# Optimization experiments

Measured on AMD Instinct MI355X. Metric: run time of the kernel, lower is better.

## Reference

```python
import jax, jax.numpy as jnp
import numpy as np

# irreps_in = 128x0e + 64x1o + 32x2e
MUL0, MUL1, MUL2 = 128, 64, 32
L1_DIM, L2_DIM = 3, 5
D0, D1, D2 = MUL0, MUL1 * L1_DIM, MUL2 * L2_DIM  # 128, 192, 160
DIM = D0 + D1 + D2                               # 480
H, Z = 64, 64
N = 16384
# fully-connected tensor-product fan-in normalization (paths: 0e*0e, 1o*1o, 2e*2e -> 0e)
ALPHA = 1.0 / np.sqrt(MUL0 * MUL0 + MUL1 * MUL1 + MUL2 * MUL2)


def setup_inputs() -> dict:
    key = jax.random.key(0)
    ks = jax.random.split(key, 8)
    return {
        "tensor_in": jax.random.normal(ks[0], (N, DIM), dtype=jnp.float32),
        "W0": jax.random.normal(ks[1], (MUL0, MUL0, H), dtype=jnp.float32),
        "W1": jax.random.normal(ks[2], (MUL1, MUL1, H), dtype=jnp.float32),
        "W2": jax.random.normal(ks[3], (MUL2, MUL2, H), dtype=jnp.float32),
        "w1": jax.random.normal(ks[4], (H, H), dtype=jnp.float32) / np.sqrt(H),
        "b1": jnp.zeros((H,), dtype=jnp.float32),
        "w2": jax.random.normal(ks[5], (H, Z), dtype=jnp.float32) / np.sqrt(H),
        "b2": jnp.zeros((Z,), dtype=jnp.float32),
        "w3": jax.random.normal(ks[6], (Z, Z), dtype=jnp.float32) / np.sqrt(Z),
        "b3": jnp.zeros((Z,), dtype=jnp.float32),
    }


def _fctp_mlp(t, W0, W1, W2, w1, b1, w2, b2, w3, b3):
    # split flat irreps vector into (mul, 2l+1) blocks
    x0 = t[:, :D0]                                   # [N, 128]    l=0
    x1 = t[:, D0:D0 + D1].reshape(-1, MUL1, L1_DIM)  # [N, 64, 3]  l=1
    x2 = t[:, D0 + D1:].reshape(-1, MUL2, L2_DIM)    # [N, 32, 5]  l=2
    # CG contraction l x l -> 0e: normalized dot over m, weighted mix over (u, v)
    h = ALPHA * (
        jnp.einsum('nu,nv,uvh->nh', x0, x0, W0)
        + jnp.einsum('num,nvm,uvh->nh', x1, x1, W1) / np.sqrt(3.0)
        + jnp.einsum('num,nvm,uvh->nh', x2, x2, W2) / np.sqrt(5.0)
    )
    h = jax.nn.silu(h @ w1 + b1)
    h = jax.nn.silu(h @ w2 + b2)
    return h @ w3 + b3                                # [N, Z]


def reference(tensor_in, W0, W1, W2, w1, b1, w2, b2, w3, b3):
    f = lambda t: _fctp_mlp(t, W0, W1, W2, w1, b1, w2, b2, w3, b3)
    x, vjp_fn = jax.vjp(f, tensor_in)
    (y,) = vjp_fn(jnp.ones_like(x))  # autograd.grad(x, tensor_in, ones_like(x))
    return x, y
```

## Files before the change

kernel.cpp:

```cpp
#include <hip/hip_runtime.h>
#include <hip/hip_bf16.h>
#include <hip/hip_fp16.h>

typedef short    bf16x8 __attribute__((ext_vector_type(8)));
typedef _Float16 f16x8  __attribute__((ext_vector_type(8)));
typedef _Float16 f16x2v __attribute__((ext_vector_type(2)));
typedef float    f32x4  __attribute__((ext_vector_type(4)));

#define DEVI __device__ __forceinline__

static constexpr int    NSAMP = 16384;
static constexpr int    TDIM  = 480;
static constexpr int    KTOT  = 21504;

static constexpr size_t SZ_B   = (size_t)KTOT * 64 * 2;
static constexpr size_t O_GWS  = 0;
static constexpr size_t O_BFWD = 0;
static constexpr size_t O_HPRE = O_BFWD + SZ_B;
static constexpr size_t O_BBWD = (size_t)TDIM * NSAMP * 4;
static constexpr size_t O_DH   = O_BBWD + SZ_B;
static constexpr size_t O_W1T  = O_DH   + (size_t)NSAMP*64*2;
static constexpr size_t O_W2T  = O_W1T + (size_t)64*64*4;
static constexpr size_t O_W3T  = O_W2T + (size_t)64*64*4;

DEVI float b2f(unsigned short s) { union { unsigned u; float f; } v; v.u = (unsigned)s << 16; return v.f; }
DEVI unsigned short f2b(float f) { union { __hip_bfloat16 h; unsigned short s; } v; v.h = __float2bfloat16(f); return v.s; }
DEVI unsigned short f2h(float f) { union { __half h; unsigned short s; } v; v.h = __float2half(f); return v.s; }
DEVI float h2f(unsigned short s) { union { unsigned short s; _Float16 h; } v; v.s = s; return (float)v.h; }
DEVI bf16x8 as_bf(uint4 q) { union { uint4 q; bf16x8 v; } u; u.q = q; return u.v; }
DEVI f16x8  as_f16(uint4 q) { union { uint4 q; f16x8 v; } u; u.q = q; return u.v; }
DEVI f32x4 mfma16(bf16x8 a, bf16x8 b, f32x4 c) { return __builtin_amdgcn_mfma_f32_16x16x32_bf16(a, b, c, 0, 0, 0); }
DEVI f32x4 mfma16h(f16x8 a, f16x8 b, f32x4 c)  { return __builtin_amdgcn_mfma_f32_16x16x32_f16 (a, b, c, 0, 0, 0); }
DEVI unsigned pkmul(unsigned a, unsigned b) {
  union { unsigned u; __half2 h; } x, y, r;
  x.u = a; y.u = b; r.h = __hmul2(x.h, y.h); return r.u;
}
DEVI unsigned pk_f16(float a, float b) {
  auto r = __builtin_amdgcn_cvt_pkrtz(a, b);
  union { decltype(r) h; unsigned u; } v;
  v.h = r; return v.u;
}
DEVI float fmix_lo(float a, unsigned w, float c) {
  float d = c;
  asm("v_fma_mix_f32 %0, %1, %2, %0 op_sel_hi:[0,1,0]" : "+v"(d) : "v"(a), "v"(w));
  return d;
}
DEVI float fmix_hi(float a, unsigned w, float c) {
  float d = c;
  asm("v_fma_mix_f32 %0, %1, %2, %0 op_sel:[0,1,0] op_sel_hi:[0,1,0]" : "+v"(d) : "v"(a), "v"(w));
  return d;
}

template<int NQ>
DEVI unsigned wsel4(const uint4 (&q)[NQ], int wi) {
  const uint4 qq = q[wi>>2];
  const int k = wi&3;
  return k==0?qq.x: k==1?qq.y: k==2?qq.z: qq.w;
}
template<int NQ>
DEVI float h16_at(const uint2 (&q)[NQ], int e) {
  const uint2 qq = q[e>>2];
  const unsigned w = ((e>>1)&1) ? qq.y : qq.x;
  const f16x2v p = __builtin_bit_cast(f16x2v, w);
  return (float)p[e&1];
}

template<int R> struct RC;
template<> struct RC<0> { static constexpr int COLS=128, OFF=0,   STRIDE=136, ROWS=128, NCH=4, NM=1, CBASE=0,   KBASE=0,    OUT=0;   };
template<> struct RC<1> { static constexpr int COLS=192, OFF=128, STRIDE=200, ROWS=64,  NCH=2, NM=3, CBASE=512, KBASE=1024, OUT=128; };
template<> struct RC<2> { static constexpr int COLS=160, OFF=320, STRIDE=168, ROWS=32,  NCH=1, NM=5, CBASE=640, KBASE=1280, OUT=320; };

__global__ __launch_bounds__(256) void k_prep(
    const float* __restrict__ W0, const float* __restrict__ W1, const float* __restrict__ W2,
    const float* __restrict__ w1, const float* __restrict__ w2, const float* __restrict__ w3,
    unsigned short* __restrict__ bfwd, unsigned short* __restrict__ bbwd,
    float* __restrict__ w1t, float* __restrict__ w2t, float* __restrict__ w3t)
{
  const int e = blockIdx.x*256 + threadIdx.x;
  const float CA = 0.0068192924f;
  const float C1 = 0.0039371205f;
  const float C2 = 0.0030496940f;
  if (e < KTOT*64) {
    {
      int j = e & 7, lane = (e>>3)&63, hf = (e>>9)&3, chunk = e>>11;
      int k = chunk*32 + (lane>>4)*8 + j;
      int h = hf*16 + (lane&15);
      float v;
      if (k < 16384)      v = CA * W0[(size_t)k*64 + h];
      else if (k < 20480) v = C1 * W1[(size_t)(k-16384)*64 + h];
      else                v = C2 * W2[(size_t)(k-20480)*64 + h];
      bfwd[e] = f2h(v);
    }
    {
      int j = e & 7, lane = (e>>3)&63, kc = (e>>9)&1, kb = e>>10;
      int k = kb*16 + (lane&15);
      int h = kc*32 + (lane>>4)*8 + j;
      float v;
      if (k < 16384)      { int u=k>>7,    vv=k&127;          v = CA*(W0[(size_t)(u*128+vv)*64+h] + W0[(size_t)(vv*128+u)*64+h]); }
      else if (k < 20480) { int l=k-16384; int u=l>>6, vv=l&63; v = C1*(W1[(size_t)(u*64+vv)*64+h] + W1[(size_t)(vv*64+u)*64+h]); }
      else                { int l=k-20480; int u=l>>5, vv=l&31; v = C2*(W2[(size_t)(u*32+vv)*64+h] + W2[(size_t)(vv*32+u)*64+h]); }
      bbwd[e] = f2b(v);
    }
  }
  if (e < 4096) {
    int i = e>>6, j = e&63;
    w1t[j*64+i] = w1[e]; w2t[j*64+i] = w2[e]; w3t[j*64+i] = w3[e];
  }
}

template<int R, bool H>
DEVI void load_tile(const float* __restrict__ t, int nb, unsigned short* lx)
{
  const int tid = threadIdx.x;
  const int s = tid >> 2, p = tid & 3;
  constexpr int CH = RC<R>::COLS/4;
  const float4* src = reinterpret_cast<const float4*>(t + (size_t)(nb+s)*TDIM + RC<R>::OFF + p*CH);
  unsigned short* dst = lx + s*RC<R>::STRIDE + p*CH;
  #pragma unroll
  for (int e4 = 0; e4 < CH/4; ++e4) {
    float4 v = src[e4];
    ushort4 o;
    if (H) { o.x = f2h(v.x); o.y = f2h(v.y); o.z = f2h(v.z); o.w = f2h(v.w); }
    else   { o.x = f2b(v.x); o.y = f2b(v.y); o.z = f2b(v.z); o.w = f2b(v.w); }
    *reinterpret_cast<ushort4*>(dst + e4*4) = o;
  }
}

DEVI void fwd_region0_f16(const unsigned short* lx, const uint4* __restrict__ bf,
                          int slot, int lane, f32x4 (&acc)[4][4])
{
  const int quad = lane>>4, col = lane&15;
  for (int u = slot; u < 128; u += 16) {
    unsigned xu2[4];
    #pragma unroll
    for (int mf = 0; mf < 4; ++mf) {
      unsigned s = lx[(mf*16+col)*136 + u];
      xu2[mf] = s | (s<<16);
    }
    #pragma unroll 1
    for (int c = 0; c < 4; ++c) {
      const int chunk = u*4 + c;
      uint4 bv[4];
      #pragma unroll
      for (int hf = 0; hf < 4; ++hf) bv[hf] = bf[(size_t)(chunk*4 + hf)*64 + lane];
      #pragma unroll
      for (int mf = 0; mf < 4; ++mf) {
        const uint4 xq = *reinterpret_cast<const uint4*>(lx + (mf*16+col)*136 + c*32 + quad*8);
        uint4 afq;
        afq.x = pkmul(xu2[mf], xq.x);
        afq.y = pkmul(xu2[mf], xq.y);
        afq.z = pkmul(xu2[mf], xq.z);
        afq.w = pkmul(xu2[mf], xq.w);
        #pragma unroll
        for (int hf = 0; hf < 4; ++hf)
          acc[mf][hf] = mfma16h(as_f16(afq), as_f16(bv[hf]), acc[mf][hf]);
      }
    }
  }
}

template<int R>
DEVI void fwd_region_f16(const unsigned short* lx, const uint4* __restrict__ bf,
                         int slot, int lane, f32x4 (&acc)[4][4])
{
  constexpr int NM = RC<R>::NM;
  const int quad = lane>>4, col = lane&15;
  for (int u = slot; u < RC<R>::ROWS; u += 16) {
    #pragma unroll 1
    for (int c = 0; c < RC<R>::NCH; ++c) {
      const int chunk = RC<R>::CBASE + u*RC<R>::NCH + c;
      uint4 bv[4];
      #pragma unroll
      for (int hf = 0; hf < 4; ++hf) bv[hf] = bf[(size_t)(chunk*4 + hf)*64 + lane];
      #pragma unroll
      for (int mf = 0; mf < 4; ++mf) {
        const unsigned short* rowp = lx + (mf*16+col)*RC<R>::STRIDE;
        float xu[NM];
        #pragma unroll
        for (int m = 0; m < NM; ++m) xu[m] = h2f(rowp[u*NM + m]);
        uint4 xq[NM];
        const uint4* xp4 = reinterpret_cast<const uint4*>(rowp + (c*32 + quad*8)*NM);
        #pragma unroll
        for (int q = 0; q < NM; ++q) xq[q] = xp4[q];
        unsigned aw[4];
        #pragma unroll
        for (int jp = 0; jp < 4; ++jp) {
          float p0 = 0.f, p1 = 0.f;
          #pragma unroll
          for (int m = 0; m < NM; ++m) {
            const int e0 = (2*jp+0)*NM + m, e1 = (2*jp+1)*NM + m;
            const unsigned w0 = wsel4(xq, e0>>1);
            const unsigned w1v = wsel4(xq, e1>>1);
            p0 = (e0&1) ? fmix_hi(xu[m], w0,  p0) : fmix_lo(xu[m], w0,  p0);
            p1 = (e1&1) ? fmix_hi(xu[m], w1v, p1) : fmix_lo(xu[m], w1v, p1);
          }
          aw[jp] = pk_f16(p0, p1);
        }
        uint4 afq; afq.x = aw[0]; afq.y = aw[1]; afq.z = aw[2]; afq.w = aw[3];
        #pragma unroll
        for (int hf = 0; hf < 4; ++hf)
          acc[mf][hf] = mfma16h(as_f16(afq), as_f16(bv[hf]), acc[mf][hf]);
      }
    }
  }
}

__global__ __launch_bounds__(256,2) void k_fwd(const float* __restrict__ t,
                                               const uint4* __restrict__ bfwd,
                                               float* __restrict__ hpre)
{
  __shared__ __align__(16) unsigned char smem[25600];
  unsigned short* lx = (unsigned short*)smem;
  const int nb = blockIdx.x*64;
  const int wv = threadIdx.x>>6, lane = threadIdx.x&63;
  const int slot = blockIdx.y*4 + wv;
  const int quad = lane>>4, col = lane&15;

  f32x4 acc[4][4];
  #pragma unroll
  for (int a = 0; a < 4; ++a)
    #pragma unroll
    for (int b = 0; b < 4; ++b) acc[a][b] = (f32x4){0.f,0.f,0.f,0.f};

  load_tile<0,true>(t, nb, lx); __syncthreads();
  fwd_region0_f16(lx, bfwd, slot, lane, acc); __syncthreads();
  load_tile<1,true>(t, nb, lx); __syncthreads();
  fwd_region_f16<1>(lx, bfwd, slot, lane, acc); __syncthreads();
  load_tile<2,true>(t, nb, lx); __syncthreads();
  fwd_region_f16<2>(lx, bfwd, slot, lane, acc); __syncthreads();

  float* red = (float*)smem;
  for (int tw = 0; tw < 4; ++tw) {
    if (wv == tw) {
      #pragma unroll
      for (int mf = 0; mf < 4; ++mf)
        #pragma unroll
        for (int hf = 0; hf < 4; ++hf)
          #pragma unroll
          for (int rr = 0; rr < 4; ++rr) {
            int idx = (mf*16 + quad*4 + rr)*64 + hf*16 + col;
            if (tw == 0) red[idx] = acc[mf][hf][rr]; else red[idx] += acc[mf][hf][rr];
          }
    }
    __syncthreads();
  }
  float* hp = hpre + (size_t)blockIdx.y*NSAMP*64;
  for (int i = threadIdx.x; i < 4096; i += 256)
    hp[(size_t)(nb + (i>>6))*64 + (i&63)] = red[i];
}

__global__ __launch_bounds__(256) void k_mlp(
    const float* __restrict__ hpre,
    const float* __restrict__ w1, const float* __restrict__ b1,
    const float* __restrict__ w2, const float* __restrict__ b2,
    const float* __restrict__ w3, const float* __restrict__ b3,
    const float* __restrict__ w1t, const float* __restrict__ w2t, const float* __restrict__ w3t,
    float* __restrict__ xout, unsigned short* __restrict__ dhb)
{
  __shared__ float Hs[64*65];
  __shared__ float Bh1[64*64];
  __shared__ float Bh2[64*64];
  __shared__ float Bg2[64*64];
  __shared__ unsigned short Bsp1[64*64];
  const int n  = threadIdx.x & 63;
  const int wv = threadIdx.x >> 6;
  const int jb = __builtin_amdgcn_readfirstlane(wv*16);
  const int nb = blockIdx.x*64;
  const size_t row = (size_t)(nb + n)*64;
  const size_t base = (size_t)nb*64;

  for (int idx = threadIdx.x; idx < 4096; idx += 256) {
    float s = hpre[base + idx]
            + hpre[(size_t)NSAMP*64   + base + idx]
            + hpre[(size_t)2*NSAMP*64 + base + idx]
            + hpre[(size_t)3*NSAMP*64 + base + idx];
    Hs[(idx>>6)*65 + (idx&63)] = s;
  }
  __syncthreads();

  float h[64];
  #pragma unroll
  for (int i = 0; i < 64; ++i) h[i] = Hs[n*65 + i];

  float dh2r[16];
  #pragma unroll
  for (int jj = 0; jj < 16; ++jj) {
    int j = jb + jj; float s = 0.f;
    #pragma unroll
    for (int z = 0; z < 64; ++z) s += w3[j*64+z];
    dh2r[jj] = s;
  }
  #pragma unroll
  for (int jj = 0; jj < 16; ++jj) {
    int j = jb + jj; float a = b1[j];
    #pragma unroll
    for (int i = 0; i < 64; ++i) a += h[i]*w1t[j*64+i];
    float sg = 1.f/(1.f + __expf(-a));
    Bh1[j*64+n] = a*sg;
    Bsp1[j*64+n] = f2b(sg*(1.f + a*(1.f-sg)));
  }
  __syncthreads();
  float h1[64];
  #pragma unroll
  for (int i = 0; i < 64; ++i) h1[i] = Bh1[i*64+n];
  #pragma unroll
  for (int jj = 0; jj < 16; ++jj) {
    int j = jb + jj; float a = b2[j];
    #pragma unroll
    for (int i = 0; i < 64; ++i) a += h1[i]*w2t[j*64+i];
    float sg = 1.f/(1.f + __expf(-a));
    Bh2[j*64+n] = a*sg;
    Bg2[j*64+n] = dh2r[jj]*(sg*(1.f + a*(1.f-sg)));
  }
  __syncthreads();
  float h2[64];
  #pragma unroll
  for (int i = 0; i < 64; ++i) h2[i] = Bh2[i*64+n];
  #pragma unroll
  for (int jj = 0; jj < 16; ++jj) {
    int j = jb + jj; float a = b3[j];
    #pragma unroll
    for (int i = 0; i < 64; ++i) a += h2[i]*w3t[j*64+i];
    xout[row + j] = a;
  }
  float g2[64];
  #pragma unroll
  for (int i = 0; i < 64; ++i) g2[i] = Bg2[i*64+n];
  #pragma unroll
  for (int jj = 0; jj < 16; ++jj) {
    int i = jb + jj; float a = 0.f;
    #pragma unroll
    for (int z = 0; z < 64; ++z) a += g2[z]*w2[i*64+z];
    Bh1[i*64+n] = a * b2f(Bsp1[i*64+n]);
  }
  __syncthreads();
  float g1[64];
  #pragma unroll
  for (int i = 0; i < 64; ++i) g1[i] = Bh1[i*64+n];
  #pragma unroll
  for (int jj = 0; jj < 16; ++jj) {
    int i = jb + jj; float a = 0.f;
    #pragma unroll
    for (int z = 0; z < 64; ++z) a += g1[z]*w1[i*64+z];
    dhb[row + i] = f2b(a);
  }
}

template<int R>
DEVI void bwd_region(const unsigned short* lx, const uint4 (&bq)[4][2],
                     const uint4* __restrict__ ba, int slot, int lane,
                     float* __restrict__ gws, int nb)
{
  constexpr int NM = RC<R>::NM;
  const int quad = lane>>4, col = lane&15;
  for (int u = slot; u < RC<R>::ROWS; u += 16) {
    float gacc[4][NM];
    #pragma unroll
    for (int nf = 0; nf < 4; ++nf)
      #pragma unroll
      for (int m = 0; m < NM; ++m) gacc[nf][m] = 0.f;

    #pragma unroll 1
    for (int c = 0; c < RC<R>::NCH; ++c) {
      uint4 aq[2][2];
      #pragma unroll
      for (int kf = 0; kf < 2; ++kf)
        #pragma unroll
        for (int kc = 0; kc < 2; ++kc) {
          int kb = RC<R>::KBASE + u*(2*RC<R>::NCH) + c*2 + kf;
          aq[kf][kc] = ba[(size_t)(kb*2+kc)*64 + lane];
        }
      #pragma unroll
      for (int kf = 0; kf < 2; ++kf) {
        const int v0 = c*32 + kf*16 + quad*4;
        #pragma unroll
        for (int nf = 0; nf < 4; ++nf) {
          f32x4 a4 = (f32x4){0.f,0.f,0.f,0.f};
          a4 = mfma16(as_bf(aq[kf][0]), as_bf(bq[nf][0]), a4);
          a4 = mfma16(as_bf(aq[kf][1]), as_bf(bq[nf][1]), a4);
          const unsigned short* xp = lx + (nf*16+col)*RC<R>::STRIDE + v0*NM;
          uint2 xq[NM];
          const uint2* xp2 = reinterpret_cast<const uint2*>(xp);
          #pragma unroll
          for (int q = 0; q < NM; ++q) xq[q] = xp2[q];
          #pragma unroll
          for (int rr = 0; rr < 4; ++rr)
            #pragma unroll
            for (int m = 0; m < NM; ++m)
              gacc[nf][m] = __builtin_fmaf(a4[rr], h16_at(xq, rr*NM + m), gacc[nf][m]);
        }
      }
    }
    #pragma unroll
    for (int nf = 0; nf < 4; ++nf)
      #pragma unroll
      for (int m = 0; m < NM; ++m) {
        float v = gacc[nf][m];
        v += __shfl_down(v, 32, 64);
        v += __shfl_down(v, 16, 64);
        if (lane < 16)
          gws[(size_t)(RC<R>::OUT + u*NM + m)*NSAMP + nb + nf*16 + lane] = v;
      }
  }
}

__global__ __launch_bounds__(256,2) void k_bwd(const float* __restrict__ t,
                                               const uint4* __restrict__ bbwd,
                                               const unsigned short* __restrict__ dh,
                                               float* __restrict__ gws)
{
  __shared__ __align__(16) unsigned char smem[25600];
  unsigned short* lx = (unsigned short*)smem;
  const int nb = blockIdx.x*64;
  const int wv = threadIdx.x>>6, lane = threadIdx.x&63;
  const int slot = blockIdx.y*4 + wv;
  const int cl = lane&15, qd = lane>>4;

  uint4 bq[4][2];
  #pragma unroll
  for (int nf = 0; nf < 4; ++nf)
    #pragma unroll
    for (int kc = 0; kc < 2; ++kc)
      bq[nf][kc] = *reinterpret_cast<const uint4*>(dh + (size_t)(nb + nf*16 + cl)*64 + kc*32 + qd*8);

  load_tile<0,true>(t, nb, lx); __syncthreads();
  bwd_region<0>(lx, bq, bbwd, slot, lane, gws, nb); __syncthreads();
  load_tile<1,true>(t, nb, lx); __syncthreads();
  bwd_region<1>(lx, bq, bbwd, slot, lane, gws, nb); __syncthreads();
  load_tile<2,true>(t, nb, lx); __syncthreads();
  bwd_region<2>(lx, bq, bbwd, slot, lane, gws, nb);
}

__global__ __launch_bounds__(256) void k_tr(const float* __restrict__ gws,
                                            float* __restrict__ y)
{
  __shared__ float tile[32][481];
  const int n0 = blockIdx.x*32;
  for (int idx = threadIdx.x; idx < 480*8; idx += 256) {
    int c = idx >> 3, i4 = idx & 7;
    float4 v = reinterpret_cast<const float4*>(gws + (size_t)c*NSAMP + n0)[i4];
    tile[i4*4+0][c] = v.x; tile[i4*4+1][c] = v.y;
    tile[i4*4+2][c] = v.z; tile[i4*4+3][c] = v.w;
  }
  __syncthreads();
  for (int idx = threadIdx.x; idx < 32*120; idx += 256) {
    int s = idx/120, c4 = idx%120;
    float4 v = { tile[s][c4*4+0], tile[s][c4*4+1], tile[s][c4*4+2], tile[s][c4*4+3] };
    reinterpret_cast<float4*>(y + (size_t)(n0+s)*TDIM)[c4] = v;
  }
}

extern "C" void kernel_launch(void* const* d_in, const int* in_sizes, int n_in,
                              void* d_out, int out_size, void* d_ws, size_t ws_size,
                              hipStream_t stream) {
  (void)in_sizes; (void)n_in; (void)out_size; (void)ws_size;
  const float* t  = (const float*)d_in[0];
  const float* W0 = (const float*)d_in[1];
  const float* W1 = (const float*)d_in[2];
  const float* W2 = (const float*)d_in[3];
  const float* w1 = (const float*)d_in[4];
  const float* b1 = (const float*)d_in[5];
  const float* w2 = (const float*)d_in[6];
  const float* b2 = (const float*)d_in[7];
  const float* w3 = (const float*)d_in[8];
  const float* b3 = (const float*)d_in[9];

  char* ws = (char*)d_ws;
  float*          gws  = (float*)(ws + O_GWS);
  unsigned short* bfwd = (unsigned short*)(ws + O_BFWD);
  unsigned short* bbwd = (unsigned short*)(ws + O_BBWD);
  float*          hpre = (float*)(ws + O_HPRE);
  unsigned short* dhb  = (unsigned short*)(ws + O_DH);
  float*          w1t  = (float*)(ws + O_W1T);
  float*          w2t  = (float*)(ws + O_W2T);
  float*          w3t  = (float*)(ws + O_W3T);

  float* xout = (float*)d_out;
  float* y    = (float*)d_out + (size_t)NSAMP*64;

  k_prep<<<dim3(5376), dim3(256), 0, stream>>>(W0, W1, W2, w1, w2, w3,
                                               bfwd, bbwd, w1t, w2t, w3t);
  k_fwd <<<dim3(256,4), dim3(256), 0, stream>>>(t, (const uint4*)bfwd, hpre);
  k_mlp <<<dim3(256), dim3(256), 0, stream>>>(hpre, w1, b1, w2, b2, w3, b3,
                                              w1t, w2t, w3t, xout, dhb);
  k_bwd <<<dim3(256,4), dim3(256), 0, stream>>>(t, (const uint4*)bbwd, dhb, gws);
  k_tr  <<<dim3(512),   dim3(256), 0, stream>>>(gws, y);
}
```

Before: 370.2 us.

## Retile MLP kernel to 16 samples per block with vectorized weight loads

The per-sample MLP kernel now handles 16 samples per block instead of 64, so 1024 blocks are launched instead of 256 and more CUs are filled. Each thread computes 4 output features rather than 16 and reads weights and LDS rows with float4 loads, using a padded row-major LDS layout. The intent is to raise parallelism and cut the per-thread serial work and scalar load count of a small kernel. The cost is that each weight row is fetched redundantly by many more blocks, and the LDS access pattern changes, which may cause bank conflicts.

```diff
diff --git a/kernel.cpp b/kernel.cpp
--- a/kernel.cpp
+++ b/kernel.cpp
@@ -257,92 +257,174 @@
     const float* __restrict__ w1t, const float* __restrict__ w2t, const float* __restrict__ w3t,
     float* __restrict__ xout, unsigned short* __restrict__ dhb)
 {
-  __shared__ float Hs[64*65];
-  __shared__ float Bh1[64*64];
-  __shared__ float Bh2[64*64];
-  __shared__ float Bg2[64*64];
-  __shared__ unsigned short Bsp1[64*64];
-  const int n  = threadIdx.x & 63;
-  const int wv = threadIdx.x >> 6;
-  const int jb = __builtin_amdgcn_readfirstlane(wv*16);
-  const int nb = blockIdx.x*64;
+  constexpr int SB  = 16;
+  constexpr int LDW = 68;
+  __shared__ float Hs [SB*LDW];
+  __shared__ float Bh1[SB*LDW];
+  __shared__ float Bh2[SB*LDW];
+  __shared__ float Bg2[SB*LDW];
+  __shared__ unsigned short Bsp1[SB*LDW];
+  const int n  = threadIdx.x & 15;
+  const int g  = threadIdx.x >> 4;
+  const int jb = g*4;
+  const int nb = blockIdx.x*SB;
   const size_t row = (size_t)(nb + n)*64;
   const size_t base = (size_t)nb*64;
 
-  for (int idx = threadIdx.x; idx < 4096; idx += 256) {
+  for (int idx = threadIdx.x; idx < SB*64; idx += 256) {
     float s = hpre[base + idx]
             + hpre[(size_t)NSAMP*64   + base + idx]
             + hpre[(size_t)2*NSAMP*64 + base + idx]
             + hpre[(size_t)3*NSAMP*64 + base + idx];
-    Hs[(idx>>6)*65 + (idx&63)] = s;
+    Hs[(idx>>6)*LDW + (idx&63)] = s;
+  }
+
+  float dh2r[4];
+  #pragma unroll
+  for (int jj = 0; jj < 4; ++jj) {
+    const float4* wr = reinterpret_cast<const float4*>(w3 + (jb+jj)*64);
+    float s = 0.f;
+    #pragma unroll
+    for (int z4 = 0; z4 < 16; ++z4) { float4 v = wr[z4]; s += v.x; s += v.y; s += v.z; s += v.w; }
+    dh2r[jj] = s;
   }
   __syncthreads();
 
-  float h[64];
+  float hrow[64];
   #pragma unroll
-  for (int i = 0; i < 64; ++i) h[i] = Hs[n*65 + i];
-
-  float dh2r[16];
+  for (int i4 = 0; i4 < 16; ++i4) {
+    float4 v = *reinterpret_cast<const float4*>(&Hs[n*LDW + i4*4]);
+    hrow[i4*4+0]=v.x; hrow[i4*4+1]=v.y; hrow[i4*4+2]=v.z; hrow[i4*4+3]=v.w;
+  }
+
+  {
+    float h1v[4], spv[4];
+    #pragma unroll
+    for (int jj = 0; jj < 4; ++jj) {
+      const int j = jb + jj;
+      float a = b1[j];
+      const float4* wr = reinterpret_cast<const float4*>(w1t + j*64);
+      #pragma unroll
+      for (int i4 = 0; i4 < 16; ++i4) {
+        float4 wv = wr[i4];
+        a += hrow[i4*4+0]*wv.x; a += hrow[i4*4+1]*wv.y;
+        a += hrow[i4*4+2]*wv.z; a += hrow[i4*4+3]*wv.w;
+      }
+      float sg = 1.f/(1.f + __expf(-a));
+      h1v[jj] = a*sg;
+      spv[jj] = sg*(1.f + a*(1.f-sg));
+    }
+    float4 o; o.x=h1v[0]; o.y=h1v[1]; o.z=h1v[2]; o.w=h1v[3];
+    *reinterpret_cast<float4*>(&Bh1[n*LDW + jb]) = o;
+    ushort4 us; us.x=f2b(spv[0]); us.y=f2b(spv[1]); us.z=f2b(spv[2]); us.w=f2b(spv[3]);
+    *reinterpret_cast<ushort4*>(&Bsp1[n*LDW + jb]) = us;
+  }
+  __syncthreads();
+
+  float h1row[64];
   #pragma unroll
-  for (int jj = 0; jj < 16; ++jj) {
-    int j = jb + jj; float s = 0.f;
-    #pragma unroll
-    for (int z = 0; z < 64; ++z) s += w3[j*64+z];
-    dh2r[jj] = s;
-  }
-  #pragma unroll
-  for (int jj = 0; jj < 16; ++jj) {
-    int j = jb + jj; float a = b1[j];
-    #pragma unroll
-    for (int i = 0; i < 64; ++i) a += h[i]*w1t[j*64+i];
-    float sg = 1.f/(1.f + __expf(-a));
-    Bh1[j*64+n] = a*sg;
-    Bsp1[j*64+n] = f2b(sg*(1.f + a*(1.f-sg)));
+  for (int i4 = 0; i4 < 16; ++i4) {
+    float4 v = *reinterpret_cast<const float4*>(&Bh1[n*LDW + i4*4]);
+    h1row[i4*4+0]=v.x; h1row[i4*4+1]=v.y; h1row[i4*4+2]=v.z; h1row[i4*4+3]=v.w;
+  }
+  {
+    float h2v[4], g2v[4];
+    #pragma unroll
+    for (int jj = 0; jj < 4; ++jj) {
+      const int j = jb + jj;
+      float a = b2[j];
+      const float4* wr = reinterpret_cast<const float4*>(w2t + j*64);
+      #pragma unroll
+      for (int i4 = 0; i4 < 16; ++i4) {
+        float4 wv = wr[i4];
+        a += h1row[i4*4+0]*wv.x; a += h1row[i4*4+1]*wv.y;
+        a += h1row[i4*4+2]*wv.z; a += h1row[i4*4+3]*wv.w;
+      }
+      float sg = 1.f/(1.f + __expf(-a));
+      h2v[jj] = a*sg;
+      g2v[jj] = dh2r[jj]*(sg*(1.f + a*(1.f-sg)));
+    }
+    float4 o; o.x=h2v[0]; o.y=h2v[1]; o.z=h2v[2]; o.w=h2v[3];
+    *reinterpret_cast<float4*>(&Bh2[n*LDW + jb]) = o;
+    float4 p; p.x=g2v[0]; p.y=g2v[1]; p.z=g2v[2]; p.w=g2v[3];
+    *reinterpret_cast<float4*>(&Bg2[n*LDW + jb]) = p;
   }
   __syncthreads();
-  float h1[64];
-  #pragma unroll
-  for (int i = 0; i < 64; ++i) h1[i] = Bh1[i*64+n];
-  #pragma unroll
-  for (int jj = 0; jj < 16; ++jj) {
-    int j = jb + jj; float a = b2[j];
-    #pragma unroll
-    for (int i = 0; i < 64; ++i) a += h1[i]*w2t[j*64+i];
-    float sg = 1.f/(1.f + __expf(-a));
-    Bh2[j*64+n] = a*sg;
-    Bg2[j*64+n] = dh2r[jj]*(sg*(1.f + a*(1.f-sg)));
+
+  {
+    float h2row[64];
+    #pragma unroll
+    for (int i4 = 0; i4 < 16; ++i4) {
+      float4 v = *reinterpret_cast<const float4*>(&Bh2[n*LDW + i4*4]);
+      h2row[i4*4+0]=v.x; h2row[i4*4+1]=v.y; h2row[i4*4+2]=v.z; h2row[i4*4+3]=v.w;
+    }
+    float xo[4];
+    #pragma unroll
+    for (int jj = 0; jj < 4; ++jj) {
+      const int j = jb + jj;
+      float a = b3[j];
+      const float4* wr = reinterpret_cast<const float4*>(w3t + j*64);
+      #pragma unroll
+      for (int i4 = 0; i4 < 16; ++i4) {
+        float4 wv = wr[i4];
+        a += h2row[i4*4+0]*wv.x; a += h2row[i4*4+1]*wv.y;
+        a += h2row[i4*4+2]*wv.z; a += h2row[i4*4+3]*wv.w;
+      }
+      xo[jj] = a;
+    }
+    float4 o; o.x=xo[0]; o.y=xo[1]; o.z=xo[2]; o.w=xo[3];
+    *reinterpret_cast<float4*>(&xout[row + jb]) = o;
+  }
+
+  {
+    float g2row[64];
+    #pragma unroll
+    for (int i4 = 0; i4 < 16; ++i4) {
+      float4 v = *reinterpret_cast<const float4*>(&Bg2[n*LDW + i4*4]);
+      g2row[i4*4+0]=v.x; g2row[i4*4+1]=v.y; g2row[i4*4+2]=v.z; g2row[i4*4+3]=v.w;
+    }
+    float g1v[4];
+    #pragma unroll
+    for (int jj = 0; jj < 4; ++jj) {
+      const int i = jb + jj;
+      float a = 0.f;
+      const float4* wr = reinterpret_cast<const float4*>(w2 + i*64);
+      #pragma unroll
+      for (int z4 = 0; z4 < 16; ++z4) {
+        float4 wv = wr[z4];
+        a += g2row[z4*4+0]*wv.x; a += g2row[z4*4+1]*wv.y;
+        a += g2row[z4*4+2]*wv.z; a += g2row[z4*4+3]*wv.w;
+      }
+      g1v[jj] = a * b2f(Bsp1[n*LDW + i]);
+    }
+    float4 o; o.x=g1v[0]; o.y=g1v[1]; o.z=g1v[2]; o.w=g1v[3];
+    *reinterpret_cast<float4*>(&Hs[n*LDW + jb]) = o;
   }
   __syncthreads();
-  float h2[64];
-  #pragma unroll
-  for (int i = 0; i < 64; ++i) h2[i] = Bh2[i*64+n];
-  #pragma unroll
-  for (int jj = 0; jj < 16; ++jj) {
-    int j = jb + jj; float a = b3[j];
-    #pragma unroll
-    for (int i = 0; i < 64; ++i) a += h2[i]*w3t[j*64+i];
-    xout[row + j] = a;
-  }
-  float g2[64];
-  #pragma unroll
-  for (int i = 0; i < 64; ++i) g2[i] = Bg2[i*64+n];
-  #pragma unroll
-  for (int jj = 0; jj < 16; ++jj) {
-    int i = jb + jj; float a = 0.f;
-    #pragma unroll
-    for (int z = 0; z < 64; ++z) a += g2[z]*w2[i*64+z];
-    Bh1[i*64+n] = a * b2f(Bsp1[i*64+n]);
-  }
-  __syncthreads();
-  float g1[64];
-  #pragma unroll
-  for (int i = 0; i < 64; ++i) g1[i] = Bh1[i*64+n];
-  #pragma unroll
-  for (int jj = 0; jj < 16; ++jj) {
-    int i = jb + jj; float a = 0.f;
-    #pragma unroll
-    for (int z = 0; z < 64; ++z) a += g1[z]*w1[i*64+z];
-    dhb[row + i] = f2b(a);
+
+  {
+    float g1row[64];
+    #pragma unroll
+    for (int i4 = 0; i4 < 16; ++i4) {
+      float4 v = *reinterpret_cast<const float4*>(&Hs[n*LDW + i4*4]);
+      g1row[i4*4+0]=v.x; g1row[i4*4+1]=v.y; g1row[i4*4+2]=v.z; g1row[i4*4+3]=v.w;
+    }
+    float dv[4];
+    #pragma unroll
+    for (int jj = 0; jj < 4; ++jj) {
+      const int i = jb + jj;
+      float a = 0.f;
+      const float4* wr = reinterpret_cast<const float4*>(w1 + i*64);
+      #pragma unroll
+      for (int z4 = 0; z4 < 16; ++z4) {
+        float4 wv = wr[z4];
+        a += g1row[z4*4+0]*wv.x; a += g1row[z4*4+1]*wv.y;
+        a += g1row[z4*4+2]*wv.z; a += g1row[z4*4+3]*wv.w;
+      }
+      dv[jj] = a;
+    }
+    ushort4 us; us.x=f2b(dv[0]); us.y=f2b(dv[1]); us.z=f2b(dv[2]); us.w=f2b(dv[3]);
+    *reinterpret_cast<ushort4*>(&dhb[row + jb]) = us;
   }
 }
 
@@ -481,8 +563,8 @@
   k_prep<<<dim3(5376), dim3(256), 0, stream>>>(W0, W1, W2, w1, w2, w3,
                                                bfwd, bbwd, w1t, w2t, w3t);
   k_fwd <<<dim3(256,4), dim3(256), 0, stream>>>(t, (const uint4*)bfwd, hpre);
-  k_mlp <<<dim3(256), dim3(256), 0, stream>>>(hpre, w1, b1, w2, b2, w3, b3,
-                                              w1t, w2t, w3t, xout, dhb);
+  k_mlp <<<dim3(1024), dim3(256), 0, stream>>>(hpre, w1, b1, w2, b2, w3, b3,
+                                               w1t, w2t, w3t, xout, dhb);
   k_bwd <<<dim3(256,4), dim3(256), 0, stream>>>(t, (const uint4*)bbwd, dhb, gws);
   k_tr  <<<dim3(512),   dim3(256), 0, stream>>>(gws, y);
 }
```

After: 314.0 us. 15.2% less time.
